# Kernel optimization log

Measured on AMD Instinct MI355X. Metric: run time of the kernel, lower is better.

The kernel has to match this reference:

```python
import jax, jax.numpy as jnp
import numpy as np

N = 50000      # nodes
E = 800000     # directed edges
D = 128        # in_dim == vertex_embed_dim
L = 3          # num_layers
EPS = 1e-5     # BatchNorm eps


def setup_inputs() -> dict:
    key = jax.random.key(0)
    k0, k1, k2 = jax.random.split(key, 3)
    x = jax.random.normal(k0, (N, D), dtype=jnp.float32)
    edge_index = jax.random.randint(k1, (2, E), 0, N, dtype=jnp.int32)
    Ws = jax.random.normal(k2, (L, D, D), dtype=jnp.float32) * 0.05
    bs = jnp.zeros((L, D), dtype=jnp.float32)
    gammas = jnp.ones((L, D), dtype=jnp.float32)
    betas = jnp.zeros((L, D), dtype=jnp.float32)
    return {"x": x, "edge_index": edge_index, "Ws": Ws, "bs": bs,
            "gammas": gammas, "betas": betas}


def reference(x, edge_index, Ws, bs, gammas, betas):
    # --- GCN normalization with self-loops (computed once, shared by all layers) ---
    loop = jnp.arange(N, dtype=edge_index.dtype)
    src = jnp.concatenate([edge_index[0], loop])   # [E+N]
    dst = jnp.concatenate([edge_index[1], loop])   # [E+N]
    deg = jax.ops.segment_sum(jnp.ones_like(dst, dtype=x.dtype), dst,
                              num_segments=N)       # in-degree of A + I
    dinv = jnp.where(deg > 0, jax.lax.rsqrt(deg), 0.0)
    norm = (dinv[src] * dinv[dst])[:, None]         # [E+N, 1]

    o = x
    h_v = [o]
    for i in range(L):
        h = o @ Ws[i]                                         # linear (no bias)
        msg = h[src] * norm                                   # gather + scale
        agg = jax.ops.segment_sum(msg, dst, num_segments=N)   # scatter-add
        agg = agg + bs[i]                                     # GCNConv bias
        # BatchNorm1d (training mode, biased batch stats)
        mu = jnp.mean(agg, axis=0)
        var = jnp.var(agg, axis=0)
        o = jax.nn.relu(gammas[i] * (agg - mu) * jax.lax.rsqrt(var + EPS)
                        + betas[i])
        h_v.append(o)
    return jnp.concatenate(h_v, axis=1)   # JK concat: [N, D*(L+1)]
```

## Files before the change

kernel.cpp:

```cpp
#include <hip/hip_runtime.h>


#define EPS_BN 1e-5f
#define NPW 2
#define REP 16

typedef short short8v __attribute__((ext_vector_type(8)));
typedef float float4v __attribute__((ext_vector_type(4)));

__device__ __forceinline__ unsigned bf16rne(float f){
  unsigned x = __float_as_uint(f);
  return (x + 0x7fffu + ((x >> 16) & 1u)) >> 16;
}
__device__ __forceinline__ float bflo(unsigned q){ return __uint_as_float(q << 16); }
__device__ __forceinline__ float bfhi(unsigned q){ return __uint_as_float(q & 0xffff0000u); }
__device__ __forceinline__ short8v as_s8(uint4 v){ return __builtin_bit_cast(short8v, v); }

__global__ void k_setup(int* __restrict__ p, int nz, int nzb,
                        const float* __restrict__ Ws, unsigned* __restrict__ Wbf){
  int b = blockIdx.x;
  if (b < nzb){
    int i = b*256 + threadIdx.x;
    if (i < nz) p[i] = 0;
  } else {
    int idx = (b - nzb)*256 + threadIdx.x;
    if (idx < 3*8192){
      int l   = idx >> 13;
      int s   = idx & 8191;
      int col = s >> 6;
      int d   = s & 3;
      int g   = ((s >> 2) & 15) ^ (col & 7);
      int kp  = g*4 + d;
      const float* W = Ws + l*16384;
      float w0 = W[(size_t)(2*kp)*128 + col];
      float w1 = W[(size_t)(2*kp+1)*128 + col];
      Wbf[idx] = bf16rne(w0) | (bf16rne(w1) << 16);
    }
  }
}

__global__ void k_scan1(const int* __restrict__ cnt, int* __restrict__ out,
                        int* __restrict__ blksum, float* __restrict__ dinv, int n){
  __shared__ int sh[256];
  int t = threadIdx.x;
  int base = blockIdx.x*1024 + t*4;
  int v[4];
  #pragma unroll
  for (int j=0;j<4;j++){
    int raw = (base+j < n) ? cnt[base+j] : 0;
    if (base+j < n) dinv[base+j] = rsqrtf((float)raw + 1.0f);
    v[j] = (base+j < n) ? ((raw + 7) & ~7) : 0;
  }
  int tsum = v[0]+v[1]+v[2]+v[3];
  sh[t] = tsum;
  __syncthreads();
  #pragma unroll
  for (int off=1; off<256; off<<=1){
    int x = (t>=off) ? sh[t-off] : 0;
    __syncthreads();
    sh[t] += x;
    __syncthreads();
  }
  if (t==255) blksum[blockIdx.x] = sh[255];
  int run = sh[t] - tsum;
  #pragma unroll
  for (int j=0;j<4;j++){ if (base+j < n) out[base+j] = run; run += v[j]; }
}

__global__ void k_scan3(int* __restrict__ out, int* __restrict__ rowcur,
                        const int* __restrict__ blksum, int nscan,
                        const int* __restrict__ cnt, int* __restrict__ colsrc, int n){
  __shared__ int lb[64];
  int t = threadIdx.x;
  if (t < nscan) lb[t] = blksum[t];
  __syncthreads();
  int i = blockIdx.x*256 + t;
  int myblk = i >> 10;
  int pre = 0, tot = 0;
  for (int k=0;k<nscan;k++){ int bv = lb[k]; tot += bv; if (k < myblk) pre += bv; }
  if (i < n){
    int r = out[i] + pre;
    out[i] = r;
    rowcur[i] = r;
    int c = cnt[i];
    int pc = (c + 7) & ~7;
    for (int p = r + c; p < r + pc; p++) colsrc[p] = 0;
  }
  if (i == 0) out[n] = tot;
}

__global__ void k_fill(const int* __restrict__ src, const int* __restrict__ dst,
                       const float* __restrict__ dinv,
                       int* __restrict__ rowcur, int* __restrict__ colsrc, int E){
  int e = blockIdx.x*256 + threadIdx.x;
  if (e < E){
    int d = dst[e];
    int pos = atomicAdd(&rowcur[d], 1);
    int s = src[e];
    colsrc[pos] = s | (int)(bf16rne(dinv[s]) << 16);
  }
}

template<int MODE>
__launch_bounds__(256)
__global__ void k_gemm(const void* __restrict__ Av, const unsigned* __restrict__ Wbf,
                       const float* __restrict__ statrep,
                       const float* __restrict__ gamma, const float* __restrict__ beta,
                       float* __restrict__ out, int colOff, unsigned* __restrict__ H2,
                       int n,
                       const int* __restrict__ dstE, int* __restrict__ cnt, int E,
                       int gemmGrid){
  const int t = threadIdx.x;
  if constexpr (MODE == 0){
    if ((int)blockIdx.x >= gemmGrid){
      int i = ((int)blockIdx.x - gemmGrid)*256 + t;
      if (i < E) atomicAdd(&cnt[dstE[i]], 1);
      return;
    }
  }
  __shared__ unsigned Wl[8192];
  __shared__ __align__(16) float ssL[256];

  if constexpr (MODE == 1){
    if (t < 128){
      float s = 0.f, s2 = 0.f;
      #pragma unroll
      for (int r=0;r<REP;r++){
        s  += statrep[r*256 + t];
        s2 += statrep[r*256 + 128 + t];
      }
      float invn = 1.0f / (float)n;
      float mu  = s * invn;
      float var = s2 * invn - mu*mu;
      float rs  = rsqrtf(var + EPS_BN);
      float sc  = gamma[t] * rs;
      ssL[t]       = sc;
      ssL[128 + t] = beta[t] - mu * sc;
    }
  }
  {
    #pragma unroll
    for (int i=0;i<8;i++){
      uint4 v = *(const uint4*)(Wbf + i*1024 + t*4);
      *(uint4*)(Wl + i*1024 + t*4) = v;
    }
  }
  __syncthreads();

  const int w  = t >> 6;
  const int l  = t & 63;
  const int lo = l & 15, hi = l >> 4;

  const int grow = blockIdx.x*64 + w*16 + lo;
  const int gr   = grow > n-1 ? n-1 : grow;
  const bool valid = grow < n;

  short8v a[4];
  #pragma unroll
  for (int kc=0;kc<4;kc++){
    const int k0 = kc*32 + hi*8;
    if constexpr (MODE == 0){
      const float4* src = (const float4*)((const float*)Av + (size_t)gr*128 + k0);
      float4 f0 = src[0], f1 = src[1];
      if (valid){
        float4* op = (float4*)(out + (size_t)grow*512 + k0);
        op[0] = f0; op[1] = f1;
      }
      uint4 pk;
      pk.x = bf16rne(f0.x) | (bf16rne(f0.y)<<16);
      pk.y = bf16rne(f0.z) | (bf16rne(f0.w)<<16);
      pk.z = bf16rne(f1.x) | (bf16rne(f1.y)<<16);
      pk.w = bf16rne(f1.z) | (bf16rne(f1.w)<<16);
      a[kc] = as_s8(pk);
    } else {
      uint4 ld = *(const uint4*)((const unsigned*)Av + (size_t)gr*64 + kc*16 + hi*4);
      float4 sc0 = *(const float4*)(ssL + k0);
      float4 sc1 = *(const float4*)(ssL + k0 + 4);
      float4 sh0 = *(const float4*)(ssL + 128 + k0);
      float4 sh1 = *(const float4*)(ssL + 128 + k0 + 4);
      float4 o0, o1;
      o0.x = fmaxf(fmaf(bflo(ld.x), sc0.x, sh0.x), 0.f);
      o0.y = fmaxf(fmaf(bfhi(ld.x), sc0.y, sh0.y), 0.f);
      o0.z = fmaxf(fmaf(bflo(ld.y), sc0.z, sh0.z), 0.f);
      o0.w = fmaxf(fmaf(bfhi(ld.y), sc0.w, sh0.w), 0.f);
      o1.x = fmaxf(fmaf(bflo(ld.z), sc1.x, sh1.x), 0.f);
      o1.y = fmaxf(fmaf(bfhi(ld.z), sc1.y, sh1.y), 0.f);
      o1.z = fmaxf(fmaf(bflo(ld.w), sc1.z, sh1.z), 0.f);
      o1.w = fmaxf(fmaf(bfhi(ld.w), sc1.w, sh1.w), 0.f);
      if (valid){
        float4* op = (float4*)(out + (size_t)grow*512 + colOff + k0);
        op[0] = o0; op[1] = o1;
      }
      uint4 pk;
      pk.x = bf16rne(o0.x) | (bf16rne(o0.y)<<16);
      pk.y = bf16rne(o0.z) | (bf16rne(o0.w)<<16);
      pk.z = bf16rne(o1.x) | (bf16rne(o1.y)<<16);
      pk.w = bf16rne(o1.z) | (bf16rne(o1.w)<<16);
      a[kc] = as_s8(pk);
    }
  }

  float4v acc[8];
  #pragma unroll
  for (int ct=0;ct<8;ct++) acc[ct] = (float4v)(0.f);

  #pragma unroll
  for (int ct=0;ct<8;ct++){
    const int col = ct*16 + lo;
    const unsigned* brow = Wl + col*64;
    const int cswz = col & 7;
    #pragma unroll
    for (int kc=0;kc<4;kc++){
      int g = (kc*4 + hi) ^ cswz;
      short8v b = *(const short8v*)(brow + g*4);
      acc[ct] = __builtin_amdgcn_mfma_f32_16x16x32_bf16(a[kc], b, acc[ct], 0, 0, 0);
    }
  }

  const int rbase = blockIdx.x*64 + w*16;
  #pragma unroll
  for (int ct=0;ct<8;ct++){
    int col = ct*16 + lo;
    #pragma unroll
    for (int r=0;r<4;r++){
      unsigned bits  = bf16rne(acc[ct][r]);
      unsigned other = (unsigned)__shfl_xor((int)bits, 1, 64);
      int gr2 = rbase + hi*4 + r;
      if (!(l & 1) && gr2 < n)
        H2[(size_t)gr2*64 + (col>>1)] = bits | (other<<16);
    }
  }
}

#define GATH(d) (*(const unsigned*)(h2c + (size_t)(unsigned)(((d)&0xffff)<<8) + lane4))
#define FMA2(d,g) { float wv_=__uint_as_float((unsigned)(d)&0xffff0000u); \
                    a0=fmaf(wv_,bflo(g),a0); a1=fmaf(wv_,bfhi(g),a1); }
__launch_bounds__(256)
__global__ void k_agg(const unsigned* __restrict__ h2, const int* __restrict__ rowptr,
                      const int* __restrict__ colsrc, const float* __restrict__ dinv,
                      unsigned* __restrict__ aggsc,
                      float* __restrict__ statrep, int n){
  __shared__ float red[4*256];
  const char* h2c = (const char*)h2;
  const int lane  = threadIdx.x & 63;
  const unsigned lane4 = lane*4;
  const int wv   = __builtin_amdgcn_readfirstlane(threadIdx.x >> 6);
  const int v0   = (blockIdx.x*4 + wv) * NPW;
  const int4* c4 = (const int4*)colsrc;
  float s0=0.f, s1=0.f, q0s=0.f, q1s=0.f;
  #pragma unroll 1
  for (int vi=0; vi<NPW; vi++){
    int v = v0 + vi;
    if (v < n){
      int j   = __builtin_amdgcn_readfirstlane(rowptr[v]);
      int end = __builtin_amdgcn_readfirstlane(rowptr[v+1]);
      unsigned qs = *(const unsigned*)(h2c + (size_t)v*256 + lane4);
      float dv = dinv[v];
      float a0 = 0.f, a1 = 0.f;
      if (j < end){
        int4 A0 = c4[(j>>2)], A1 = c4[(j>>2)+1];
        unsigned g0=GATH(A0.x), g1=GATH(A0.y), g2=GATH(A0.z), g3=GATH(A0.w);
        unsigned g4=GATH(A1.x), g5=GATH(A1.y), g6=GATH(A1.z), g7=GATH(A1.w);
        #pragma unroll 1
        for (;;){
          int jn = j + 8;
          bool more = jn < end;
          int4 B0, B1;
          unsigned p0,p1,p2,p3,p4,p5,p6,p7;
          if (more){
            B0 = c4[(jn>>2)]; B1 = c4[(jn>>2)+1];
            p0=GATH(B0.x); p1=GATH(B0.y); p2=GATH(B0.z); p3=GATH(B0.w);
            p4=GATH(B1.x); p5=GATH(B1.y); p6=GATH(B1.z); p7=GATH(B1.w);
          }
          FMA2(A0.x,g0) FMA2(A0.y,g1) FMA2(A0.z,g2) FMA2(A0.w,g3)
          FMA2(A1.x,g4) FMA2(A1.y,g5) FMA2(A1.z,g6) FMA2(A1.w,g7)
          if (!more) break;
          A0=B0; A1=B1;
          g0=p0; g1=p1; g2=p2; g3=p3; g4=p4; g5=p5; g6=p6; g7=p7;
          j = jn;
        }
      }
      a0 = dv*(a0 + dv*bflo(qs));
      a1 = dv*(a1 + dv*bfhi(qs));
      aggsc[(size_t)v*64 + lane] = bf16rne(a0) | (bf16rne(a1) << 16);
      s0 += a0; q0s = fmaf(a0,a0,q0s);
      s1 += a1; q1s = fmaf(a1,a1,q1s);
    }
  }
  red[wv*256 + 2*lane]       = s0;
  red[wv*256 + 2*lane+1]     = s1;
  red[wv*256 + 128+2*lane]   = q0s;
  red[wv*256 + 128+2*lane+1] = q1s;
  __syncthreads();
  int t = threadIdx.x;
  float tot = red[t] + red[256+t] + red[512+t] + red[768+t];
  atomicAdd(&statrep[((blockIdx.x & (REP-1))<<8) + t], tot);
}

__launch_bounds__(256)
__global__ void k_bnfinal(const unsigned* __restrict__ aggsc,
                          const float* __restrict__ statrep,
                          const float* __restrict__ gamma, const float* __restrict__ beta,
                          float* __restrict__ out, int colOff, int n){
  __shared__ float ssL[256];
  int t = threadIdx.x;
  if (t < 128){
    float s = 0.f, s2 = 0.f;
    #pragma unroll
    for (int r=0;r<REP;r++){
      s  += statrep[r*256 + t];
      s2 += statrep[r*256 + 128 + t];
    }
    float invn = 1.0f / (float)n;
    float mu  = s * invn;
    float var = s2 * invn - mu*mu;
    float rs  = rsqrtf(var + EPS_BN);
    float sc  = gamma[t] * rs;
    ssL[t]       = sc;
    ssL[128 + t] = beta[t] - mu * sc;
  }
  __syncthreads();
  int i = blockIdx.x*256 + t;
  if (i >= n*16) return;
  int v = i >> 4, c = i & 15;
  uint4 ld = *(const uint4*)(aggsc + (size_t)v*64 + c*4);
  int k0 = c*8;
  float4 o0, o1;
  o0.x = fmaxf(fmaf(bflo(ld.x), ssL[k0+0], ssL[128+k0+0]), 0.f);
  o0.y = fmaxf(fmaf(bfhi(ld.x), ssL[k0+1], ssL[128+k0+1]), 0.f);
  o0.z = fmaxf(fmaf(bflo(ld.y), ssL[k0+2], ssL[128+k0+2]), 0.f);
  o0.w = fmaxf(fmaf(bfhi(ld.y), ssL[k0+3], ssL[128+k0+3]), 0.f);
  o1.x = fmaxf(fmaf(bflo(ld.z), ssL[k0+4], ssL[128+k0+4]), 0.f);
  o1.y = fmaxf(fmaf(bfhi(ld.z), ssL[k0+5], ssL[128+k0+5]), 0.f);
  o1.z = fmaxf(fmaf(bflo(ld.w), ssL[k0+6], ssL[128+k0+6]), 0.f);
  o1.w = fmaxf(fmaf(bfhi(ld.w), ssL[k0+7], ssL[128+k0+7]), 0.f);
  float4* op = (float4*)(out + (size_t)v*512 + colOff + k0);
  op[0] = o0; op[1] = o1;
}

extern "C" void kernel_launch(void* const* d_in, const int* in_sizes, int n_in,
                              void* d_out, int out_size, void* d_ws, size_t ws_size,
                              hipStream_t stream){
  const float* x      = (const float*)d_in[0];
  const int*   ei     = (const int*)d_in[1];
  const float* Ws     = (const float*)d_in[2];
  const float* gammas = (const float*)d_in[4];
  const float* betas  = (const float*)d_in[5];
  const int N = in_sizes[0] / 128;
  const int E = in_sizes[1] / 2;
  float* out = (float*)d_out;

  const int EPADCAP = E + 7*N + 8;

  char* w = (char*)d_ws;
  auto alloc = [&](size_t bytes)->char*{
    char* p = w; w += (bytes + 255) & ~(size_t)255; return p;
  };
  int*      cnt     = (int*)     alloc((size_t)N*4);
  float*    statrep = (float*)   alloc(3*REP*256*4);
  int*      rowptr  = (int*)     alloc((size_t)(N+1)*4);
  int*      rowcur  = (int*)     alloc((size_t)N*4);
  int*      blksum  = (int*)     alloc(64*4);
  int*      colsrc  = (int*)     alloc((size_t)EPADCAP*4);
  float*    dinv    = (float*)   alloc((size_t)N*4);
  unsigned* Wbf     = (unsigned*)alloc(3*8192*4);
  unsigned* h2      = (unsigned*)alloc((size_t)N*64*4);
  unsigned* aggsc   = (unsigned*)alloc((size_t)N*64*4);

  const int* srcArr = ei;
  const int* dstArr = ei + E;

  const int nbN = (N + 255)/256;
  const int nbE = (E + 255)/256;
  const int nscan = (N + 1023)/1024;
  const int nz  = (int)(((char*)statrep - (char*)cnt)/4) + 3*REP*256;
  const int nzb = (nz + 255)/256;
  const int nwp = (3*8192 + 255)/256;

  const int gemmGrid = (N + 63)/64;
  const int aggGrid  = (N + 4*NPW-1)/(4*NPW);

  k_setup<<<nzb + nwp,256,0,stream>>>(cnt, nz, nzb, Ws, Wbf);
  k_gemm<0><<<gemmGrid + nbE,256,0,stream>>>(x, Wbf, nullptr, nullptr, nullptr,
                                             out, 0, h2, N,
                                             dstArr, cnt, E, gemmGrid);
  k_scan1<<<nscan,256,0,stream>>>(cnt, rowptr, blksum, dinv, N);
  k_scan3<<<nbN,256,0,stream>>>(rowptr, rowcur, blksum, nscan, cnt, colsrc, N);
  k_fill<<<nbE,256,0,stream>>>(srcArr, dstArr, dinv, rowcur, colsrc, E);

  for (int l=0; l<3; l++){
    if (l > 0)
      k_gemm<1><<<gemmGrid,256,0,stream>>>(aggsc, Wbf + l*8192,
                                           statrep + (l-1)*REP*256,
                                           gammas + (l-1)*128, betas + (l-1)*128,
                                           out, l*128, h2, N,
                                           nullptr, nullptr, 0, gemmGrid);
    k_agg<<<aggGrid,256,0,stream>>>(h2, rowptr, colsrc, dinv, aggsc,
                                    statrep + l*REP*256, N);
  }
  k_bnfinal<<<(N*16 + 255)/256,256,0,stream>>>(aggsc, statrep + 2*REP*256,
                                               gammas + 2*128, betas + 2*128,
                                               out, 3*128, N);
}
```

Measured before the change: 233.8 us.

## Split feature matrix into column quarters for cache-local aggregation gathers

Stores the bf16 hidden features and aggregated outputs in four column-quarter planes of 64 bytes per node, and launches four times as many aggregation blocks, each handling one quarter. Within a wave, four slots each take every fourth edge, and partial sums are combined with shuffles. The intent is to shrink the per-pass gather working set so it stays in cache, and to use nontemporal stores for the output. In exchange, edge indices are re-read four times, each gather fetches only 64 bytes, and the kernel adds shuffle reductions.

```diff
diff --git a/kernel.cpp b/kernel.cpp
--- a/kernel.cpp
+++ b/kernel.cpp
@@ -2,7 +2,6 @@
 
 
 #define EPS_BN 1e-5f
-#define NPW 2
 #define REP 16
 
 typedef short short8v __attribute__((ext_vector_type(8)));
@@ -15,6 +14,7 @@
 __device__ __forceinline__ float bflo(unsigned q){ return __uint_as_float(q << 16); }
 __device__ __forceinline__ float bfhi(unsigned q){ return __uint_as_float(q & 0xffff0000u); }
 __device__ __forceinline__ short8v as_s8(uint4 v){ return __builtin_bit_cast(short8v, v); }
+__device__ __forceinline__ float4v as_f4(float4 v){ return __builtin_bit_cast(float4v, v); }
 
 __global__ void k_setup(int* __restrict__ p, int nz, int nzb,
                         const float* __restrict__ Ws, unsigned* __restrict__ Wbf){
@@ -120,6 +120,7 @@
   }
   __shared__ unsigned Wl[8192];
   __shared__ __align__(16) float ssL[256];
+  const size_t qstride = (size_t)n*16;
 
   if constexpr (MODE == 1){
     if (t < 128){
@@ -163,8 +164,9 @@
       const float4* src = (const float4*)((const float*)Av + (size_t)gr*128 + k0);
       float4 f0 = src[0], f1 = src[1];
       if (valid){
-        float4* op = (float4*)(out + (size_t)grow*512 + k0);
-        op[0] = f0; op[1] = f1;
+        float4v* op = (float4v*)(out + (size_t)grow*512 + k0);
+        __builtin_nontemporal_store(as_f4(f0), op);
+        __builtin_nontemporal_store(as_f4(f1), op+1);
       }
       uint4 pk;
       pk.x = bf16rne(f0.x) | (bf16rne(f0.y)<<16);
@@ -173,23 +175,20 @@
       pk.w = bf16rne(f1.z) | (bf16rne(f1.w)<<16);
       a[kc] = as_s8(pk);
     } else {
-      uint4 ld = *(const uint4*)((const unsigned*)Av + (size_t)gr*64 + kc*16 + hi*4);
-      float4 sc0 = *(const float4*)(ssL + k0);
-      float4 sc1 = *(const float4*)(ssL + k0 + 4);
-      float4 sh0 = *(const float4*)(ssL + 128 + k0);
-      float4 sh1 = *(const float4*)(ssL + 128 + k0 + 4);
+      uint4 ld = *(const uint4*)((const unsigned*)Av + (size_t)kc*qstride + (size_t)gr*16 + hi*4);
       float4 o0, o1;
-      o0.x = fmaxf(fmaf(bflo(ld.x), sc0.x, sh0.x), 0.f);
-      o0.y = fmaxf(fmaf(bfhi(ld.x), sc0.y, sh0.y), 0.f);
-      o0.z = fmaxf(fmaf(bflo(ld.y), sc0.z, sh0.z), 0.f);
-      o0.w = fmaxf(fmaf(bfhi(ld.y), sc0.w, sh0.w), 0.f);
-      o1.x = fmaxf(fmaf(bflo(ld.z), sc1.x, sh1.x), 0.f);
-      o1.y = fmaxf(fmaf(bfhi(ld.z), sc1.y, sh1.y), 0.f);
-      o1.z = fmaxf(fmaf(bflo(ld.w), sc1.z, sh1.z), 0.f);
-      o1.w = fmaxf(fmaf(bfhi(ld.w), sc1.w, sh1.w), 0.f);
+      o0.x = fmaxf(fmaf(bflo(ld.x), ssL[k0+0], ssL[128+k0+0]), 0.f);
+      o0.y = fmaxf(fmaf(bfhi(ld.x), ssL[k0+1], ssL[128+k0+1]), 0.f);
+      o0.z = fmaxf(fmaf(bflo(ld.y), ssL[k0+2], ssL[128+k0+2]), 0.f);
+      o0.w = fmaxf(fmaf(bfhi(ld.y), ssL[k0+3], ssL[128+k0+3]), 0.f);
+      o1.x = fmaxf(fmaf(bflo(ld.z), ssL[k0+4], ssL[128+k0+4]), 0.f);
+      o1.y = fmaxf(fmaf(bfhi(ld.z), ssL[k0+5], ssL[128+k0+5]), 0.f);
+      o1.z = fmaxf(fmaf(bflo(ld.w), ssL[k0+6], ssL[128+k0+6]), 0.f);
+      o1.w = fmaxf(fmaf(bfhi(ld.w), ssL[k0+7], ssL[128+k0+7]), 0.f);
       if (valid){
-        float4* op = (float4*)(out + (size_t)grow*512 + colOff + k0);
-        op[0] = o0; op[1] = o1;
+        float4v* op = (float4v*)(out + (size_t)grow*512 + colOff + k0);
+        __builtin_nontemporal_store(as_f4(o0), op);
+        __builtin_nontemporal_store(as_f4(o1), op+1);
       }
       uint4 pk;
       pk.x = bf16rne(o0.x) | (bf16rne(o0.y)<<16);
@@ -226,75 +225,82 @@
       unsigned bits  = bf16rne(acc[ct][r]);
       unsigned other = (unsigned)__shfl_xor((int)bits, 1, 64);
       int gr2 = rbase + hi*4 + r;
-      if (!(l & 1) && gr2 < n)
-        H2[(size_t)gr2*64 + (col>>1)] = bits | (other<<16);
-    }
-  }
-}
-
-#define GATH(d) (*(const unsigned*)(h2c + (size_t)(unsigned)(((d)&0xffff)<<8) + lane4))
-#define FMA2(d,g) { float wv_=__uint_as_float((unsigned)(d)&0xffff0000u); \
-                    a0=fmaf(wv_,bflo(g),a0); a1=fmaf(wv_,bfhi(g),a1); }
+      if (!(l & 1) && gr2 < n){
+        int colp = col >> 1;
+        H2[(size_t)(colp>>4)*qstride + (size_t)gr2*16 + (colp&15)] = bits | (other<<16);
+      }
+    }
+  }
+}
+
 __launch_bounds__(256)
 __global__ void k_agg(const unsigned* __restrict__ h2, const int* __restrict__ rowptr,
-                      const int* __restrict__ colsrc, const float* __restrict__ dinv,
+                      const unsigned* __restrict__ colsrc, const float* __restrict__ dinv,
                       unsigned* __restrict__ aggsc,
-                      float* __restrict__ statrep, int n){
-  __shared__ float red[4*256];
-  const char* h2c = (const char*)h2;
-  const int lane  = threadIdx.x & 63;
-  const unsigned lane4 = lane*4;
-  const int wv   = __builtin_amdgcn_readfirstlane(threadIdx.x >> 6);
-  const int v0   = (blockIdx.x*4 + wv) * NPW;
-  const int4* c4 = (const int4*)colsrc;
+                      float* __restrict__ statrep, int n, int ngrpq){
+  __shared__ float red[1024];
+  const int bid = blockIdx.x;
+  const int q   = bid / ngrpq;
+  const int blk = bid - q*ngrpq;
+  const int t    = threadIdx.x;
+  const int lane = t & 63;
+  const int wv   = t >> 6;
+  const int f    = lane & 15;
+  const int slot = lane >> 4;
+  const size_t qstride = (size_t)n*16;
+  const unsigned* h2q = h2 + (size_t)q*qstride;
+
   float s0=0.f, s1=0.f, q0s=0.f, q1s=0.f;
   #pragma unroll 1
-  for (int vi=0; vi<NPW; vi++){
-    int v = v0 + vi;
+  for (int vi=0; vi<2; vi++){
+    int v = (blk*4 + wv)*2 + vi;
     if (v < n){
-      int j   = __builtin_amdgcn_readfirstlane(rowptr[v]);
+      int beg = __builtin_amdgcn_readfirstlane(rowptr[v]);
       int end = __builtin_amdgcn_readfirstlane(rowptr[v+1]);
-      unsigned qs = *(const unsigned*)(h2c + (size_t)v*256 + lane4);
       float dv = dinv[v];
+      unsigned qs = h2q[(size_t)v*16 + f];
       float a0 = 0.f, a1 = 0.f;
-      if (j < end){
-        int4 A0 = c4[(j>>2)], A1 = c4[(j>>2)+1];
-        unsigned g0=GATH(A0.x), g1=GATH(A0.y), g2=GATH(A0.z), g3=GATH(A0.w);
-        unsigned g4=GATH(A1.x), g5=GATH(A1.y), g6=GATH(A1.z), g7=GATH(A1.w);
+      int chunks = (end - beg) >> 2;
+      if (chunks > 0){
+        const unsigned* cp = colsrc + beg + slot;
+        unsigned e0 = __builtin_nontemporal_load(cp);
+        unsigned e1 = (chunks > 1) ? __builtin_nontemporal_load(cp + 4) : 0u;
+        unsigned g0 = h2q[(size_t)(e0 & 0xffffu)*16 + f];
         #pragma unroll 1
-        for (;;){
-          int jn = j + 8;
-          bool more = jn < end;
-          int4 B0, B1;
-          unsigned p0,p1,p2,p3,p4,p5,p6,p7;
-          if (more){
-            B0 = c4[(jn>>2)]; B1 = c4[(jn>>2)+1];
-            p0=GATH(B0.x); p1=GATH(B0.y); p2=GATH(B0.z); p3=GATH(B0.w);
-            p4=GATH(B1.x); p5=GATH(B1.y); p6=GATH(B1.z); p7=GATH(B1.w);
-          }
-          FMA2(A0.x,g0) FMA2(A0.y,g1) FMA2(A0.z,g2) FMA2(A0.w,g3)
-          FMA2(A1.x,g4) FMA2(A1.y,g5) FMA2(A1.z,g6) FMA2(A1.w,g7)
-          if (!more) break;
-          A0=B0; A1=B1;
-          g0=p0; g1=p1; g2=p2; g3=p3; g4=p4; g5=p5; g6=p6; g7=p7;
-          j = jn;
+        for (int c=0;;){
+          unsigned e2 = 0u, g1 = 0u;
+          if (c+2 < chunks) e2 = __builtin_nontemporal_load(cp + 4*(c+2));
+          if (c+1 < chunks) g1 = h2q[(size_t)(e1 & 0xffffu)*16 + f];
+          float wv_ = __uint_as_float(e0 & 0xffff0000u);
+          a0 = fmaf(wv_, bflo(g0), a0);
+          a1 = fmaf(wv_, bfhi(g0), a1);
+          if (++c >= chunks) break;
+          e0 = e1; e1 = e2; g0 = g1;
         }
       }
+      a0 += __shfl_xor(a0, 16, 64);  a1 += __shfl_xor(a1, 16, 64);
+      a0 += __shfl_xor(a0, 32, 64);  a1 += __shfl_xor(a1, 32, 64);
       a0 = dv*(a0 + dv*bflo(qs));
       a1 = dv*(a1 + dv*bfhi(qs));
-      aggsc[(size_t)v*64 + lane] = bf16rne(a0) | (bf16rne(a1) << 16);
-      s0 += a0; q0s = fmaf(a0,a0,q0s);
-      s1 += a1; q1s = fmaf(a1,a1,q1s);
-    }
-  }
-  red[wv*256 + 2*lane]       = s0;
-  red[wv*256 + 2*lane+1]     = s1;
-  red[wv*256 + 128+2*lane]   = q0s;
-  red[wv*256 + 128+2*lane+1] = q1s;
+      if (slot == 0){
+        aggsc[(size_t)q*qstride + (size_t)v*16 + f] = bf16rne(a0) | (bf16rne(a1) << 16);
+        s0 += a0; q0s = fmaf(a0,a0,q0s);
+        s1 += a1; q1s = fmaf(a1,a1,q1s);
+      }
+    }
+  }
+  if (slot == 0){
+    red[wv*256 + q*32 + 2*f]         = s0;
+    red[wv*256 + q*32 + 2*f + 1]     = s1;
+    red[wv*256 + 128 + q*32 + 2*f]     = q0s;
+    red[wv*256 + 128 + q*32 + 2*f + 1] = q1s;
+  }
   __syncthreads();
-  int t = threadIdx.x;
-  float tot = red[t] + red[256+t] + red[512+t] + red[768+t];
-  atomicAdd(&statrep[((blockIdx.x & (REP-1))<<8) + t], tot);
+  if (t < 64){
+    int j = (t < 32) ? (q*32 + t) : (128 + q*32 + (t - 32));
+    float tot = red[j] + red[256+j] + red[512+j] + red[768+j];
+    atomicAdd(&statrep[((bid & (REP-1))<<8) + j], tot);
+  }
 }
 
 __launch_bounds__(256)
@@ -304,6 +310,7 @@
                           float* __restrict__ out, int colOff, int n){
   __shared__ float ssL[256];
   int t = threadIdx.x;
+  const size_t qstride = (size_t)n*16;
   if (t < 128){
     float s = 0.f, s2 = 0.f;
     #pragma unroll
@@ -323,7 +330,7 @@
   int i = blockIdx.x*256 + t;
   if (i >= n*16) return;
   int v = i >> 4, c = i & 15;
-  uint4 ld = *(const uint4*)(aggsc + (size_t)v*64 + c*4);
+  uint4 ld = *(const uint4*)(aggsc + (size_t)(c>>2)*qstride + (size_t)v*16 + (c&3)*4);
   int k0 = c*8;
   float4 o0, o1;
   o0.x = fmaxf(fmaf(bflo(ld.x), ssL[k0+0], ssL[128+k0+0]), 0.f);
@@ -334,8 +341,9 @@
   o1.y = fmaxf(fmaf(bfhi(ld.z), ssL[k0+5], ssL[128+k0+5]), 0.f);
   o1.z = fmaxf(fmaf(bflo(ld.w), ssL[k0+6], ssL[128+k0+6]), 0.f);
   o1.w = fmaxf(fmaf(bfhi(ld.w), ssL[k0+7], ssL[128+k0+7]), 0.f);
-  float4* op = (float4*)(out + (size_t)v*512 + colOff + k0);
-  op[0] = o0; op[1] = o1;
+  float4v* op = (float4v*)(out + (size_t)v*512 + colOff + k0);
+  __builtin_nontemporal_store(as_f4(o0), op);
+  __builtin_nontemporal_store(as_f4(o1), op+1);
 }
 
 extern "C" void kernel_launch(void* const* d_in, const int* in_sizes, int n_in,
@@ -350,7 +358,7 @@
   const int E = in_sizes[1] / 2;
   float* out = (float*)d_out;
 
-  const int EPADCAP = E + 7*N + 8;
+  const int EPADCAP = E + 7*N + 64;
 
   char* w = (char*)d_ws;
   auto alloc = [&](size_t bytes)->char*{
@@ -378,7 +386,8 @@
   const int nwp = (3*8192 + 255)/256;
 
   const int gemmGrid = (N + 63)/64;
-  const int aggGrid  = (N + 4*NPW-1)/(4*NPW);
+  const int ngrpq    = (N + 7)/8;
+  const int aggGrid  = 4*ngrpq;
 
   k_setup<<<nzb + nwp,256,0,stream>>>(cnt, nz, nzb, Ws, Wbf);
   k_gemm<0><<<gemmGrid + nbE,256,0,stream>>>(x, Wbf, nullptr, nullptr, nullptr,
@@ -395,8 +404,8 @@
                                            gammas + (l-1)*128, betas + (l-1)*128,
                                            out, l*128, h2, N,
                                            nullptr, nullptr, 0, gemmGrid);
-    k_agg<<<aggGrid,256,0,stream>>>(h2, rowptr, colsrc, dinv, aggsc,
-                                    statrep + l*REP*256, N);
+    k_agg<<<aggGrid,256,0,stream>>>(h2, rowptr, (const unsigned*)colsrc, dinv, aggsc,
+                                    statrep + l*REP*256, N, ngrpq);
   }
   k_bnfinal<<<(N*16 + 255)/256,256,0,stream>>>(aggsc, statrep + 2*REP*256,
                                                gammas + 2*128, betas + 2*128,
```

Result: slower. 409.0 us (+74.9%).
